# Kernel tuning notes

Hardware: AMD Instinct MI355X
Metric: run time of the kernel (lower is better)

## Reference

```python
import jax, jax.numpy as jnp
import numpy as np

K = 1024
D = 256
BETA = 0.25


def setup_inputs() -> dict:
    key = jax.random.key(0)
    k1, k2 = jax.random.split(key)
    z = jax.random.normal(k1, (32, D, 32, 32), dtype=jnp.float32)
    # embedding initialized uniform(-1/K, 1/K) as in the torch module
    emb = jax.random.uniform(k2, (K, D), minval=-1.0 / K, maxval=1.0 / K,
                             dtype=jnp.float32)
    return {"z": z, "emb": emb}


def reference(z, emb):
    B, _, H, W = z.shape
    z_nhwc = jnp.transpose(z, (0, 2, 3, 1))          # [B, H, W, D]
    zf = z_nhwc.reshape(-1, D)                        # [N, D]
    # squared euclidean distance: ||z||^2 + ||e||^2 - 2 z e^T
    d = (jnp.sum(zf * zf, axis=1, keepdims=True)
         + jnp.sum(emb * emb, axis=1)
         - 2.0 * jnp.matmul(zf, emb.T))               # [N, K]
    idx = jnp.argmin(d, axis=1)                       # [N]
    min_encodings = jax.nn.one_hot(idx, K, dtype=z.dtype)  # [N, K]
    # direct gather instead of one_hot @ emb (same math)
    z_q = emb[idx].reshape(z_nhwc.shape)              # [B, H, W, D]
    sg = jax.lax.stop_gradient
    loss = (jnp.mean((sg(z_q) - z_nhwc) ** 2)
            + BETA * jnp.mean((z_q - sg(z_nhwc)) ** 2))
    # straight-through estimator
    z_q_st = z_nhwc + sg(z_q - z_nhwc)
    e_mean = jnp.mean(min_encodings, axis=0)          # [K]
    perplexity = jnp.exp(-jnp.sum(e_mean * jnp.log(e_mean + 1e-10)))
    z_q_out = jnp.transpose(z_q_st, (0, 3, 1, 2))     # [B, D, H, W]
    return (loss, z_q_out, perplexity, min_encodings,
            idx.reshape(B, H, W))
```

## Files before the change

kernel.cpp:

```cpp
#include <hip/hip_runtime.h>
#include <math.h>

#define K_CODES 1024
#define D_DIM   256
#define HW      1024
#define N_ROWS  32768
#define TAU     1.2e-4f

typedef __attribute__((ext_vector_type(8))) short bf16x8;
typedef __attribute__((ext_vector_type(4))) float f32x4;
#define MFMA16(a, b, c) __builtin_amdgcn_mfma_f32_16x16x32_bf16(a, b, c, 0, 0, 0)

__device__ __forceinline__ unsigned bf16_rne_bits(float x) {
    unsigned u = __float_as_uint(x);
    return (u + 0x7FFFu + ((u >> 16) & 1u)) >> 16;
}

__device__ __forceinline__ float pw_block128_sq(const float* a) {
    #pragma clang fp contract(off)
    float S[16];
    #pragma unroll
    for (int l = 0; l < 16; ++l) {
        float x0 = a[l],      x4 = a[64 + l];
        float x1 = a[16 + l], x5 = a[80 + l];
        float x2 = a[32 + l], x6 = a[96 + l];
        float x3 = a[48 + l], x7 = a[112 + l];
        float r0 = x0 * x0 + x4 * x4;
        float r1 = x1 * x1 + x5 * x5;
        float r2 = x2 * x2 + x6 * x6;
        float r3 = x3 * x3 + x7 * x7;
        S[l] = (r0 + r1) + (r2 + r3);
    }
    float u0 = S[0] + S[8],  u1 = S[1] + S[9],  u2 = S[2] + S[10], u3 = S[3] + S[11];
    float u4 = S[4] + S[12], u5 = S[5] + S[13], u6 = S[6] + S[14], u7 = S[7] + S[15];
    float v0 = u0 + u4, v1 = u1 + u5, v2 = u2 + u6, v3 = u3 + u7;
    return (v0 + v2) + (v1 + v3);
}
__device__ __forceinline__ float pw_sum256_sq(const float* a) {
    #pragma clang fp contract(off)
    float b0 = pw_block128_sq(a);
    float b1 = pw_block128_sq(a + 128);
    return b0 + b1;
}

__global__ void k_emb_cvt(const float* __restrict__ emb,
                          ushort* __restrict__ hi, ushort* __restrict__ lo) {
    int i = blockIdx.x * 256 + threadIdx.x;
    float4 v = reinterpret_cast<const float4*>(emb)[i];
    ushort4 h, l;
    float x[4] = {v.x, v.y, v.z, v.w};
    ushort hb[4], lb[4];
    #pragma unroll
    for (int j = 0; j < 4; ++j) {
        unsigned hbits = bf16_rne_bits(x[j]);
        float hf = __uint_as_float(hbits << 16);
        unsigned lbits = bf16_rne_bits(x[j] - hf);
        hb[j] = (ushort)hbits; lb[j] = (ushort)lbits;
    }
    h.x = hb[0]; h.y = hb[1]; h.z = hb[2]; h.w = hb[3];
    l.x = lb[0]; l.y = lb[1]; l.z = lb[2]; l.w = lb[3];
    reinterpret_cast<ushort4*>(hi)[i] = h;
    reinterpret_cast<ushort4*>(lo)[i] = l;
}

__global__ void k_emb_norm(const float* __restrict__ emb, float* __restrict__ enorm) {
    int k = blockIdx.x * 256 + threadIdx.x;
    if (k < K_CODES) enorm[k] = pw_sum256_sq(emb + (size_t)k * D_DIM);
}

#define BT_STR 264
#define BT_BLK (16 * BT_STR)
__global__ __launch_bounds__(256, 2) void k_screen_mfma(
    const float* __restrict__ z,
    const ushort* __restrict__ emb_hi, const ushort* __restrict__ emb_lo,
    const float* __restrict__ enorm, float* __restrict__ zn_row,
    int* __restrict__ idx_ws, int* __restrict__ worklist,
    int* __restrict__ hardlist, int* __restrict__ nflag)
{
    __shared__ __align__(16) float zl[64 * 257];
    __shared__ float enorm_lds[K_CODES];
    __shared__ float zn_sh[64];

    const int tid  = threadIdx.x;
    const int lane = tid & 63, wave = tid >> 6;
    const int blk  = blockIdx.x;
    const int batch = blk >> 4;
    const int p0    = (blk & 15) * 64;
    const float* zb = z + (size_t)batch * D_DIM * HW;

    {
        int p = tid & 63;
        for (int d = tid >> 6; d < D_DIM; d += 4)
            zl[p * 257 + d] = zb[(size_t)d * HW + p0 + p];
    }
    for (int i = tid; i < K_CODES; i += 256) enorm_lds[i] = enorm[i];
    __syncthreads();

    if (tid < 64) {
        float zn = pw_sum256_sq(&zl[tid * 257]);
        zn_sh[tid] = zn;
        zn_row[blk * 64 + tid] = zn;
    }

    const int fr = lane & 15, fg = lane >> 4;
    bf16x8 Ah[8], Al[8];
    {
        const float* zr = &zl[(wave * 16 + fr) * 257];
        #pragma unroll
        for (int s = 0; s < 8; ++s) {
            int c0 = s * 32 + fg * 8;
            bf16x8 h, l;
            #pragma unroll
            for (int j = 0; j < 8; ++j) {
                float x = zr[c0 + j];
                unsigned hb = bf16_rne_bits(x);
                float hf = __uint_as_float(hb << 16);
                unsigned lb = bf16_rne_bits(x - hf);
                h[j] = (short)hb; l[j] = (short)lb;
            }
            Ah[s] = h; Al[s] = l;
        }
    }
    __syncthreads();

    ushort* bt = reinterpret_cast<ushort*>(zl);

    auto stage = [&](int buf, int kt) {
        int row = tid >> 5, d16 = tid & 31;
        #pragma unroll
        for (int i = 0; i < 2; ++i) {
            int r = row + 8 * i;
            size_t src = ((size_t)(kt * 16 + r) << 8) + d16 * 8;
            uint4 vh = *reinterpret_cast<const uint4*>(emb_hi + src);
            uint4 vl = *reinterpret_cast<const uint4*>(emb_lo + src);
            *reinterpret_cast<uint4*>(&bt[(buf * 2 + 0) * BT_BLK + r * BT_STR + d16 * 8]) = vh;
            *reinterpret_cast<uint4*>(&bt[(buf * 2 + 1) * BT_BLK + r * BT_STR + d16 * 8]) = vl;
        }
    };

    float zn4[4];
    #pragma unroll
    for (int r = 0; r < 4; ++r) zn4[r] = zn_sh[wave * 16 + fg * 4 + r];

    float b1v[4] = {1e30f, 1e30f, 1e30f, 1e30f};
    float b2v[4] = {1e30f, 1e30f, 1e30f, 1e30f};
    float b3v[4] = {1e30f, 1e30f, 1e30f, 1e30f};
    int   b1i[4] = {0, 0, 0, 0};
    int   b2i[4] = {0, 0, 0, 0};

    stage(0, 0);
    __syncthreads();

    const int boff = fr * BT_STR + fg * 8;
    for (int kt = 0; kt < 64; ++kt) {
        int cur = kt & 1;
        if (kt < 63) stage(cur ^ 1, kt + 1);

        f32x4 aHH = {0.f, 0.f, 0.f, 0.f};
        f32x4 aHM = {0.f, 0.f, 0.f, 0.f};
        f32x4 aLH = {0.f, 0.f, 0.f, 0.f};
        const ushort* bhp = bt + cur * 2 * BT_BLK + boff;
        const ushort* blp = bhp + BT_BLK;
        #pragma unroll
        for (int s = 0; s < 8; ++s) {
            bf16x8 Bh = *reinterpret_cast<const bf16x8*>(bhp + s * 32);
            bf16x8 Bl = *reinterpret_cast<const bf16x8*>(blp + s * 32);
            aHH = MFMA16(Ah[s], Bh, aHH);
            aHM = MFMA16(Ah[s], Bl, aHM);
            aLH = MFMA16(Al[s], Bh, aLH);
        }
        {
            #pragma clang fp contract(off)
            float en = enorm_lds[kt * 16 + fr];
            int kk = kt * 16 + fr;
            #pragma unroll
            for (int r = 0; r < 4; ++r) {
                float m  = aHH[r] + (aHM[r] + aLH[r]);
                float t1 = zn4[r] + en;
                float s  = t1 - 2.0f * m;
                if (s < b1v[r]) {
                    b3v[r] = b2v[r];
                    b2v[r] = b1v[r]; b2i[r] = b1i[r];
                    b1v[r] = s;      b1i[r] = kk;
                } else if (s < b2v[r]) {
                    b3v[r] = b2v[r];
                    b2v[r] = s;      b2i[r] = kk;
                } else if (s < b3v[r]) {
                    b3v[r] = s;
                }
            }
        }
        __syncthreads();
    }

    const int n0w = blk * 64 + wave * 16;
    #pragma unroll
    for (int r = 0; r < 4; ++r) {
        float v1 = b1v[r]; int i1 = b1i[r];
        float v2 = b2v[r]; int i2 = b2i[r];
        float v3 = b3v[r];
        #pragma unroll
        for (int o = 8; o >= 1; o >>= 1) {
            float ov1 = __shfl_xor(v1, o); int oi1 = __shfl_xor(i1, o);
            float ov2 = __shfl_xor(v2, o); int oi2 = __shfl_xor(i2, o);
            float ov3 = __shfl_xor(v3, o);
            bool t1 = (ov1 < v1) || (ov1 == v1 && oi1 < i1);
            float w1  = t1 ? ov1 : v1;  int wi1 = t1 ? oi1 : i1;
            float l1  = t1 ? v1  : ov1; int li1 = t1 ? i1  : oi1;
            float wv2 = t1 ? ov2 : v2;  int wi2 = t1 ? oi2 : i2;
            float wv3 = t1 ? ov3 : v3;
            float lv2 = t1 ? v2  : ov2;
            bool t2 = (wv2 < l1) || (wv2 == l1 && wi2 < li1);
            float m2 = t2 ? wv2 : l1;   int mi2 = t2 ? wi2 : li1;
            float m3 = t2 ? fminf(wv3, l1) : fminf(wv2, lv2);
            v1 = w1; i1 = wi1; v2 = m2; i2 = mi2; v3 = m3;
        }
        if (fr == 0) {
            int n = n0w + fg * 4 + r;
            idx_ws[n] = i1;
            if (v3 - v1 <= TAU) {
                int slot = atomicAdd(&nflag[1], 1);
                hardlist[slot] = n;
            } else if (v2 - v1 <= TAU) {
                int slot = atomicAdd(&nflag[0], 1);
                worklist[slot] = n | (i2 << 16);
            }
        }
    }
}

__global__ __launch_bounds__(256) void k_epilogue(
    const float* __restrict__ z, const float* __restrict__ emb,
    const int* __restrict__ idx_ws,
    float* __restrict__ zq_out, float* __restrict__ idxf_out,
    float* __restrict__ enc, float* __restrict__ loss_row,
    int* __restrict__ counts)
{
    __shared__ int kb[64];
    __shared__ float lpart[4][64];
    const int tid = threadIdx.x;
    const int blk = blockIdx.x;
    const int batch = blk >> 4;
    const int p0 = (blk & 15) * 64;
    const int n0 = blk * 64;

    if (tid < 64) {
        int k = idx_ws[n0 + tid];
        kb[tid] = k;
        idxf_out[n0 + tid] = (float)k;
        enc[(size_t)(n0 + tid) * K_CODES + k] = 1.0f;
        atomicAdd(&counts[k], 1);
    }
    __syncthreads();

    int p = tid & 63, dg = tid >> 6;
    const float* zp = z + (size_t)batch * D_DIM * HW + p0 + p;
    float* zqp = zq_out + (size_t)batch * D_DIM * HW + p0 + p;
    const float* er = emb + (size_t)kb[p] * D_DIM;
    float ls = 0.0f;
    for (int d = dg * 64; d < dg * 64 + 64; ++d) {
        float e = er[d];
        float zv = zp[(size_t)d * HW];
        float df = e - zv;
        ls += df * df;
        zqp[(size_t)d * HW] = e;
    }
    lpart[dg][p] = ls;
    __syncthreads();
    if (tid < 64)
        loss_row[n0 + tid] = (lpart[0][tid] + lpart[1][tid]) + (lpart[2][tid] + lpart[3][tid]);
}

__global__ __launch_bounds__(256) void k_pairfix(
    const float* __restrict__ z, const float* __restrict__ emb,
    const float* __restrict__ enorm, const float* __restrict__ zn_row,
    const int* __restrict__ worklist, const int* __restrict__ nflag,
    int* __restrict__ idx_ws, int* __restrict__ counts,
    float* __restrict__ loss_row, float* __restrict__ zq_out,
    float* __restrict__ idxf_out, float* __restrict__ enc)
{
    const int lane = threadIdx.x & 63;
    const int gw = blockIdx.x * 4 + (threadIdx.x >> 6);
    const int nw = gridDim.x * 4;
    const int nf = nflag[0];

    for (int j = gw; j < nf; j += nw) {
        const int e  = worklist[j];
        const int n  = e & 0xFFFF;
        const int i2 = e >> 16;
        const int i1 = idx_ws[n];
        const int batch = n >> 10, p = n & (HW - 1);
        const float* zp = z + (size_t)batch * D_DIM * HW + p;

        float zr[4], e1[4], e2[4];
        #pragma unroll
        for (int i = 0; i < 4; ++i) {
            int d = lane + 64 * i;
            zr[i] = zp[(size_t)d * HW];
            e1[i] = emb[(size_t)i1 * D_DIM + d];
            e2[i] = emb[(size_t)i2 * D_DIM + d];
        }
        double p1 = ((double)zr[0] * (double)e1[0] + (double)zr[1] * (double)e1[1])
                  + ((double)zr[2] * (double)e1[2] + (double)zr[3] * (double)e1[3]);
        double p2 = ((double)zr[0] * (double)e2[0] + (double)zr[1] * (double)e2[1])
                  + ((double)zr[2] * (double)e2[2] + (double)zr[3] * (double)e2[3]);
        #pragma unroll
        for (int o = 1; o <= 32; o <<= 1) {
            p1 += __shfl_xor(p1, o);
            p2 += __shfl_xor(p2, o);
        }
        float s1, s2;
        {
            #pragma clang fp contract(off)
            float zn = zn_row[n];
            float mf1 = (float)p1, mf2 = (float)p2;
            s1 = (zn + enorm[i1]) - 2.0f * mf1;
            s2 = (zn + enorm[i2]) - 2.0f * mf2;
        }
        const bool swap = (s2 < s1) || (s2 == s1 && i2 < i1);
        if (swap) {
            float lsum = 0.0f;
            float* zqp = zq_out + (size_t)batch * D_DIM * HW + p;
            #pragma unroll
            for (int i = 0; i < 4; ++i) {
                int d = lane + 64 * i;
                float df = e2[i] - zr[i];
                lsum += df * df;
                zqp[(size_t)d * HW] = e2[i];
            }
            #pragma unroll
            for (int o = 32; o >= 1; o >>= 1) lsum += __shfl_xor(lsum, o);
            if (lane == 0) {
                loss_row[n] = lsum;
                idx_ws[n] = i2;
                idxf_out[n] = (float)i2;
                enc[(size_t)n * K_CODES + i1] = 0.0f;
                enc[(size_t)n * K_CODES + i2] = 1.0f;
                atomicSub(&counts[i1], 1);
                atomicAdd(&counts[i2], 1);
            }
        }
    }
}

__global__ __launch_bounds__(256, 4) void k_hard(
    const float* __restrict__ z, const float* __restrict__ emb,
    const float* __restrict__ enorm, const float* __restrict__ zn_row,
    const int* __restrict__ hardlist, const int* __restrict__ nflag,
    int* __restrict__ idx_ws, int* __restrict__ counts,
    float* __restrict__ loss_row, float* __restrict__ zq_out,
    float* __restrict__ idxf_out, float* __restrict__ enc)
{
    __shared__ __align__(16) float zrow[D_DIM];
    __shared__ float wv[4]; __shared__ int wi[4];
    __shared__ int fi_sh;

    const int tid  = threadIdx.x;
    const int lane = tid & 63, wave = tid >> 6;
    const int slot = tid >> 2, qt = tid & 3;
    const int nf = nflag[1];

    for (int j = blockIdx.x; j < nf; j += gridDim.x) {
        const int n = hardlist[j];
        const int batch = n >> 10, p = n & (HW - 1);

        zrow[tid] = z[(size_t)batch * D_DIM * HW + (size_t)tid * HW + p];
        __syncthreads();

        float bv = 1e30f; int bi = 0;
        const float znr = zn_row[n];
        const float* zq4 = &zrow[qt * 64];

        for (int pp = 0; pp < 16; ++pp) {
            const int c = pp * 64 + slot;
            const float* er = emb + (size_t)c * D_DIM + qt * 64;
            double a0 = 0.0, a1 = 0.0, a2 = 0.0, a3 = 0.0;
            #pragma unroll
            for (int d = 0; d < 64; d += 4) {
                float4 e4 = *reinterpret_cast<const float4*>(er + d);
                float4 z4 = *reinterpret_cast<const float4*>(zq4 + d);
                a0 += (double)z4.x * (double)e4.x;
                a1 += (double)z4.y * (double)e4.y;
                a2 += (double)z4.z * (double)e4.z;
                a3 += (double)z4.w * (double)e4.w;
            }
            double part = (a0 + a1) + (a2 + a3);
            part += __shfl_xor(part, 1);
            part += __shfl_xor(part, 2);
            {
                #pragma clang fp contract(off)
                float mf = (float)part;
                float t1 = znr + enorm[c];
                float s  = t1 - 2.0f * mf;
                if (qt == 0) {
                    if (s < bv) { bv = s; bi = c; }
                }
            }
        }
        if (qt != 0) bv = 1e30f;

        #pragma unroll
        for (int o = 32; o >= 1; o >>= 1) {
            float ov = __shfl_xor(bv, o);
            int   oi = __shfl_xor(bi, o);
            if (ov < bv || (ov == bv && oi < bi)) { bv = ov; bi = oi; }
        }
        if (lane == 0) { wv[wave] = bv; wi[wave] = bi; }
        __syncthreads();
        if (tid == 0) {
            float fv = wv[0]; int fi = wi[0];
            #pragma unroll
            for (int w = 1; w < 4; ++w)
                if (wv[w] < fv || (wv[w] == fv && wi[w] < fi)) { fv = wv[w]; fi = wi[w]; }
            fi_sh = fi;
        }
        __syncthreads();

        const int fi = fi_sh;
        const int old = idx_ws[n];
        if (fi != old && wave == 0) {
            float lsum = 0.0f;
            float* zqp = zq_out + (size_t)batch * D_DIM * HW + p;
            #pragma unroll
            for (int i = 0; i < 4; ++i) {
                int d = lane + 64 * i;
                float e = emb[(size_t)fi * D_DIM + d];
                float df = e - zrow[d];
                lsum += df * df;
                zqp[(size_t)d * HW] = e;
            }
            #pragma unroll
            for (int o = 32; o >= 1; o >>= 1) lsum += __shfl_xor(lsum, o);
            if (lane == 0) {
                loss_row[n] = lsum;
                idx_ws[n] = fi;
                idxf_out[n] = (float)fi;
                enc[(size_t)n * K_CODES + old] = 0.0f;
                enc[(size_t)n * K_CODES + fi] = 1.0f;
                atomicSub(&counts[old], 1);
                atomicAdd(&counts[fi], 1);
            }
        }
        __syncthreads();
    }
}

__global__ void k_final(const float* __restrict__ loss_row,
                        const int* __restrict__ counts,
                        float* __restrict__ out_loss, float* __restrict__ out_perp) {
    __shared__ float la[4], pa[4];
    int tid = threadIdx.x;
    float ls = 0.0f, ps = 0.0f;
    for (int i = tid; i < N_ROWS; i += 256) ls += loss_row[i];
    for (int i = tid; i < K_CODES; i += 256) {
        float em = (float)counts[i] * (1.0f / (float)N_ROWS);
        ps += em * logf(em + 1e-10f);
    }
    #pragma unroll
    for (int off = 32; off > 0; off >>= 1) {
        ls += __shfl_down(ls, off);
        ps += __shfl_down(ps, off);
    }
    if ((tid & 63) == 0) { la[tid >> 6] = ls; pa[tid >> 6] = ps; }
    __syncthreads();
    if (tid == 0) {
        float L = (la[0] + la[1] + la[2] + la[3]) * (1.25f / (float)((size_t)N_ROWS * D_DIM));
        float P = expf(-(pa[0] + pa[1] + pa[2] + pa[3]));
        *out_loss = L;
        *out_perp = P;
    }
}

extern "C" void kernel_launch(void* const* d_in, const int* in_sizes, int n_in,
                              void* d_out, int out_size, void* d_ws, size_t ws_size,
                              hipStream_t stream) {
    const float* z   = (const float*)d_in[0];
    const float* emb = (const float*)d_in[1];
    float* out = (float*)d_out;

    float* out_loss = out;
    float* out_zq   = out + 1;
    float* out_perp = out + 1 + (size_t)N_ROWS * D_DIM;
    float* out_enc  = out_perp + 1;
    float* out_idxf = out_enc + (size_t)N_ROWS * K_CODES;

    char* ws = (char*)d_ws;
    int*    idx_ws   = (int*)(ws + 0);
    int*    counts   = (int*)(ws + 131072);
    float*  enorm    = (float*)(ws + 135168);
    float*  loss_row = (float*)(ws + 139264);
    int*    worklist = (int*)(ws + 270336);
    int*    nflag    = (int*)(ws + 401408);
    ushort* emb_hi   = (ushort*)(ws + 401664);
    ushort* emb_lo   = (ushort*)(ws + 925952);
    float*  zn_row   = (float*)(ws + 1450240);
    int*    hardlist = (int*)(ws + 1581312);

    hipMemsetAsync(counts, 0, K_CODES * sizeof(int), stream);
    hipMemsetAsync(nflag, 0, 2 * sizeof(int), stream);
    hipMemsetAsync(out_enc, 0, (size_t)N_ROWS * K_CODES * sizeof(float), stream);

    k_emb_cvt<<<256, 256, 0, stream>>>(emb, emb_hi, emb_lo);
    k_emb_norm<<<(K_CODES + 255) / 256, 256, 0, stream>>>(emb, enorm);
    k_screen_mfma<<<512, 256, 0, stream>>>(z, emb_hi, emb_lo, enorm, zn_row,
                                           idx_ws, worklist, hardlist, nflag);
    k_epilogue<<<512, 256, 0, stream>>>(z, emb, idx_ws, out_zq, out_idxf,
                                        out_enc, loss_row, counts);
    k_pairfix<<<128, 256, 0, stream>>>(z, emb, enorm, zn_row, worklist, nflag,
                                       idx_ws, counts, loss_row, out_zq,
                                       out_idxf, out_enc);
    k_hard<<<64, 256, 0, stream>>>(z, emb, enorm, zn_row, hardlist, nflag,
                                   idx_ws, counts, loss_row, out_zq,
                                   out_idxf, out_enc);
    k_final<<<1, 256, 0, stream>>>(loss_row, counts, out_loss, out_perp);
}
```

Baseline: 326.2 us.

## Double rows per screen block to reuse staged codebook tiles across two row groups

New measurement: 346.3 us. 1.06x slower.

```diff
diff --git a/kernel.cpp b/kernel.cpp
--- a/kernel.cpp
+++ b/kernel.cpp
@@ -68,44 +68,46 @@
     if (k < K_CODES) enorm[k] = pw_sum256_sq(emb + (size_t)k * D_DIM);
 }
 
-#define BT_STR 264
+#define SROWS 128
+#define BT_STR 280
 #define BT_BLK (16 * BT_STR)
-__global__ __launch_bounds__(256, 2) void k_screen_mfma(
+__global__ __launch_bounds__(256, 1) void k_screen_mfma(
     const float* __restrict__ z,
     const ushort* __restrict__ emb_hi, const ushort* __restrict__ emb_lo,
     const float* __restrict__ enorm, float* __restrict__ zn_row,
     int* __restrict__ idx_ws, int* __restrict__ worklist,
     int* __restrict__ hardlist, int* __restrict__ nflag)
 {
-    __shared__ __align__(16) float zl[64 * 257];
+    __shared__ __align__(16) float zl[SROWS * 257];
     __shared__ float enorm_lds[K_CODES];
-    __shared__ float zn_sh[64];
+    __shared__ float zn_sh[SROWS];
 
     const int tid  = threadIdx.x;
     const int lane = tid & 63, wave = tid >> 6;
     const int blk  = blockIdx.x;
-    const int batch = blk >> 4;
-    const int p0    = (blk & 15) * 64;
+    const int batch = blk >> 3;
+    const int p0    = (blk & 7) * SROWS;
     const float* zb = z + (size_t)batch * D_DIM * HW;
 
     {
-        int p = tid & 63;
-        for (int d = tid >> 6; d < D_DIM; d += 4)
+        int p = tid & 127;
+        for (int d = tid >> 7; d < D_DIM; d += 2)
             zl[p * 257 + d] = zb[(size_t)d * HW + p0 + p];
     }
     for (int i = tid; i < K_CODES; i += 256) enorm_lds[i] = enorm[i];
     __syncthreads();
 
-    if (tid < 64) {
+    if (tid < SROWS) {
         float zn = pw_sum256_sq(&zl[tid * 257]);
         zn_sh[tid] = zn;
-        zn_row[blk * 64 + tid] = zn;
+        zn_row[blk * SROWS + tid] = zn;
     }
 
     const int fr = lane & 15, fg = lane >> 4;
-    bf16x8 Ah[8], Al[8];
-    {
-        const float* zr = &zl[(wave * 16 + fr) * 257];
+    bf16x8 Ah[2][8], Al[2][8];
+    #pragma unroll
+    for (int rg = 0; rg < 2; ++rg) {
+        const float* zr = &zl[(wave * 32 + rg * 16 + fr) * 257];
         #pragma unroll
         for (int s = 0; s < 8; ++s) {
             int c0 = s * 32 + fg * 8;
@@ -118,7 +120,7 @@
                 unsigned lb = bf16_rne_bits(x - hf);
                 h[j] = (short)hb; l[j] = (short)lb;
             }
-            Ah[s] = h; Al[s] = l;
+            Ah[rg][s] = h; Al[rg][s] = l;
         }
     }
     __syncthreads();
@@ -138,15 +140,22 @@
         }
     };
 
-    float zn4[4];
-    #pragma unroll
-    for (int r = 0; r < 4; ++r) zn4[r] = zn_sh[wave * 16 + fg * 4 + r];
-
-    float b1v[4] = {1e30f, 1e30f, 1e30f, 1e30f};
-    float b2v[4] = {1e30f, 1e30f, 1e30f, 1e30f};
-    float b3v[4] = {1e30f, 1e30f, 1e30f, 1e30f};
-    int   b1i[4] = {0, 0, 0, 0};
-    int   b2i[4] = {0, 0, 0, 0};
+    float zn4[2][4];
+    #pragma unroll
+    for (int rg = 0; rg < 2; ++rg)
+        #pragma unroll
+        for (int r = 0; r < 4; ++r)
+            zn4[rg][r] = zn_sh[wave * 32 + rg * 16 + fg * 4 + r];
+
+    float b1v[2][4], b2v[2][4], b3v[2][4];
+    int   b1i[2][4], b2i[2][4];
+    #pragma unroll
+    for (int rg = 0; rg < 2; ++rg)
+        #pragma unroll
+        for (int r = 0; r < 4; ++r) {
+            b1v[rg][r] = 1e30f; b2v[rg][r] = 1e30f; b3v[rg][r] = 1e30f;
+            b1i[rg][r] = 0;     b2i[rg][r] = 0;
+        }
 
     stage(0, 0);
     __syncthreads();
@@ -156,49 +165,59 @@
         int cur = kt & 1;
         if (kt < 63) stage(cur ^ 1, kt + 1);
 
-        f32x4 aHH = {0.f, 0.f, 0.f, 0.f};
-        f32x4 aHM = {0.f, 0.f, 0.f, 0.f};
-        f32x4 aLH = {0.f, 0.f, 0.f, 0.f};
+        f32x4 aHH[2], aHM[2], aLH[2];
+        #pragma unroll
+        for (int rg = 0; rg < 2; ++rg) {
+            aHH[rg] = (f32x4){0.f, 0.f, 0.f, 0.f};
+            aHM[rg] = (f32x4){0.f, 0.f, 0.f, 0.f};
+            aLH[rg] = (f32x4){0.f, 0.f, 0.f, 0.f};
+        }
         const ushort* bhp = bt + cur * 2 * BT_BLK + boff;
         const ushort* blp = bhp + BT_BLK;
         #pragma unroll
         for (int s = 0; s < 8; ++s) {
             bf16x8 Bh = *reinterpret_cast<const bf16x8*>(bhp + s * 32);
             bf16x8 Bl = *reinterpret_cast<const bf16x8*>(blp + s * 32);
-            aHH = MFMA16(Ah[s], Bh, aHH);
-            aHM = MFMA16(Ah[s], Bl, aHM);
-            aLH = MFMA16(Al[s], Bh, aLH);
+            #pragma unroll
+            for (int rg = 0; rg < 2; ++rg) {
+                aHH[rg] = MFMA16(Ah[rg][s], Bh, aHH[rg]);
+                aHM[rg] = MFMA16(Ah[rg][s], Bl, aHM[rg]);
+                aLH[rg] = MFMA16(Al[rg][s], Bh, aLH[rg]);
+            }
         }
         {
             #pragma clang fp contract(off)
             float en = enorm_lds[kt * 16 + fr];
             int kk = kt * 16 + fr;
             #pragma unroll
-            for (int r = 0; r < 4; ++r) {
-                float m  = aHH[r] + (aHM[r] + aLH[r]);
-                float t1 = zn4[r] + en;
-                float s  = t1 - 2.0f * m;
-                if (s < b1v[r]) {
-                    b3v[r] = b2v[r];
-                    b2v[r] = b1v[r]; b2i[r] = b1i[r];
-                    b1v[r] = s;      b1i[r] = kk;
-                } else if (s < b2v[r]) {
-                    b3v[r] = b2v[r];
-                    b2v[r] = s;      b2i[r] = kk;
-                } else if (s < b3v[r]) {
-                    b3v[r] = s;
+            for (int rg = 0; rg < 2; ++rg)
+                #pragma unroll
+                for (int r = 0; r < 4; ++r) {
+                    float m  = aHH[rg][r] + (aHM[rg][r] + aLH[rg][r]);
+                    float t1 = zn4[rg][r] + en;
+                    float s  = t1 - 2.0f * m;
+                    if (s < b1v[rg][r]) {
+                        b3v[rg][r] = b2v[rg][r];
+                        b2v[rg][r] = b1v[rg][r]; b2i[rg][r] = b1i[rg][r];
+                        b1v[rg][r] = s;          b1i[rg][r] = kk;
+                    } else if (s < b2v[rg][r]) {
+                        b3v[rg][r] = b2v[rg][r];
+                        b2v[rg][r] = s;          b2i[rg][r] = kk;
+                    } else if (s < b3v[rg][r]) {
+                        b3v[rg][r] = s;
+                    }
                 }
-            }
         }
         __syncthreads();
     }
 
-    const int n0w = blk * 64 + wave * 16;
+    #pragma unroll
+    for (int rg = 0; rg < 2; ++rg)
     #pragma unroll
     for (int r = 0; r < 4; ++r) {
-        float v1 = b1v[r]; int i1 = b1i[r];
-        float v2 = b2v[r]; int i2 = b2i[r];
-        float v3 = b3v[r];
+        float v1 = b1v[rg][r]; int i1 = b1i[rg][r];
+        float v2 = b2v[rg][r]; int i2 = b2i[rg][r];
+        float v3 = b3v[rg][r];
         #pragma unroll
         for (int o = 8; o >= 1; o >>= 1) {
             float ov1 = __shfl_xor(v1, o); int oi1 = __shfl_xor(i1, o);
@@ -216,7 +235,7 @@
             v1 = w1; i1 = wi1; v2 = m2; i2 = mi2; v3 = m3;
         }
         if (fr == 0) {
-            int n = n0w + fg * 4 + r;
+            int n = blk * SROWS + wave * 32 + rg * 16 + fg * 4 + r;
             idx_ws[n] = i1;
             if (v3 - v1 <= TAU) {
                 int slot = atomicAdd(&nflag[1], 1);
@@ -502,7 +521,7 @@
 
     k_emb_cvt<<<256, 256, 0, stream>>>(emb, emb_hi, emb_lo);
     k_emb_norm<<<(K_CODES + 255) / 256, 256, 0, stream>>>(emb, enorm);
-    k_screen_mfma<<<512, 256, 0, stream>>>(z, emb_hi, emb_lo, enorm, zn_row,
+    k_screen_mfma<<<256, 256, 0, stream>>>(z, emb_hi, emb_lo, enorm, zn_row,
                                            idx_ws, worklist, hardlist, nflag);
     k_epilogue<<<512, 256, 0, stream>>>(z, emb, idx_ws, out_zq, out_idxf,
                                         out_enc, loss_row, counts);
```

## Stream codebook tiles via direct global-to-LDS loads with 4-deep XOR-swizzled ring

Applied to the files above, without the earlier changes.

After: 327.9 us. No clear change (+0.5%).

```diff
diff --git a/kernel.cpp b/kernel.cpp
--- a/kernel.cpp
+++ b/kernel.cpp
@@ -68,8 +68,6 @@
     if (k < K_CODES) enorm[k] = pw_sum256_sq(emb + (size_t)k * D_DIM);
 }
 
-#define BT_STR 264
-#define BT_BLK (16 * BT_STR)
 __global__ __launch_bounds__(256, 2) void k_screen_mfma(
     const float* __restrict__ z,
     const ushort* __restrict__ emb_hi, const ushort* __restrict__ emb_lo,
@@ -121,26 +119,33 @@
             Ah[s] = h; Al[s] = l;
         }
     }
-    __syncthreads();
-
-    ushort* bt = reinterpret_cast<ushort*>(zl);
-
-    auto stage = [&](int buf, int kt) {
-        int row = tid >> 5, d16 = tid & 31;
-        #pragma unroll
-        for (int i = 0; i < 2; ++i) {
-            int r = row + 8 * i;
-            size_t src = ((size_t)(kt * 16 + r) << 8) + d16 * 8;
-            uint4 vh = *reinterpret_cast<const uint4*>(emb_hi + src);
-            uint4 vl = *reinterpret_cast<const uint4*>(emb_lo + src);
-            *reinterpret_cast<uint4*>(&bt[(buf * 2 + 0) * BT_BLK + r * BT_STR + d16 * 8]) = vh;
-            *reinterpret_cast<uint4*>(&bt[(buf * 2 + 1) * BT_BLK + r * BT_STR + d16 * 8]) = vl;
-        }
-    };
-
     float zn4[4];
     #pragma unroll
     for (int r = 0; r < 4; ++r) zn4[r] = zn_sh[wave * 16 + fg * 4 + r];
+    __syncthreads();
+
+    ushort* bt = reinterpret_cast<ushort*>(zl);
+    const int fr7 = fr & 7;
+
+    auto issue_tile = [&](int kt) {
+        int buf = kt & 3;
+        #pragma unroll
+        for (int h = 0; h < 2; ++h) {
+            const ushort* sb = h ? emb_lo : emb_hi;
+            #pragma unroll
+            for (int i = 0; i < 2; ++i) {
+                int r0 = wave * 4 + i * 2;
+                int r  = r0 + (lane >> 5);
+                int u  = (lane & 31) ^ (r & 7);
+                const ushort* src = sb + ((size_t)(kt * 16 + r) << 8) + u * 8;
+                ushort* dst = bt + buf * 8192 + h * 4096 + r0 * 256;
+                __builtin_amdgcn_global_load_lds(
+                    (const __attribute__((address_space(1))) void*)src,
+                    (__attribute__((address_space(3))) void*)dst,
+                    16, 0, 0);
+            }
+        }
+    };
 
     float b1v[4] = {1e30f, 1e30f, 1e30f, 1e30f};
     float b2v[4] = {1e30f, 1e30f, 1e30f, 1e30f};
@@ -148,23 +153,25 @@
     int   b1i[4] = {0, 0, 0, 0};
     int   b2i[4] = {0, 0, 0, 0};
 
-    stage(0, 0);
-    __syncthreads();
-
-    const int boff = fr * BT_STR + fg * 8;
+    issue_tile(0); issue_tile(1); issue_tile(2);
+
     for (int kt = 0; kt < 64; ++kt) {
-        int cur = kt & 1;
-        if (kt < 63) stage(cur ^ 1, kt + 1);
-
+        if (kt < 62)      asm volatile("s_waitcnt vmcnt(8)" ::: "memory");
+        else if (kt == 62) asm volatile("s_waitcnt vmcnt(4)" ::: "memory");
+        else               asm volatile("s_waitcnt vmcnt(0)" ::: "memory");
+        __builtin_amdgcn_s_barrier();
+        asm volatile("" ::: "memory");
+        if (kt < 61) issue_tile(kt + 3);
+
+        const ushort* bb = bt + (kt & 3) * 8192 + fr * 256;
         f32x4 aHH = {0.f, 0.f, 0.f, 0.f};
         f32x4 aHM = {0.f, 0.f, 0.f, 0.f};
         f32x4 aLH = {0.f, 0.f, 0.f, 0.f};
-        const ushort* bhp = bt + cur * 2 * BT_BLK + boff;
-        const ushort* blp = bhp + BT_BLK;
         #pragma unroll
         for (int s = 0; s < 8; ++s) {
-            bf16x8 Bh = *reinterpret_cast<const bf16x8*>(bhp + s * 32);
-            bf16x8 Bl = *reinterpret_cast<const bf16x8*>(blp + s * 32);
+            int u = (s * 4 + fg) ^ fr7;
+            bf16x8 Bh = *reinterpret_cast<const bf16x8*>(bb + u * 8);
+            bf16x8 Bl = *reinterpret_cast<const bf16x8*>(bb + 4096 + u * 8);
             aHH = MFMA16(Ah[s], Bh, aHH);
             aHM = MFMA16(Ah[s], Bl, aHM);
             aLH = MFMA16(Al[s], Bh, aLH);
@@ -190,7 +197,6 @@
                 }
             }
         }
-        __syncthreads();
     }
 
     const int n0w = blk * 64 + wave * 16;
```
